# Kernel tuning notes

Hardware: AMD Instinct MI355X
Metric: run time of the kernel (lower is better)

The kernel has to match this reference:

```python
import jax, jax.numpy as jnp
import numpy as np

B, L, D, H, S = 2, 2048, 1024, 16, 4
Dh = D // H
EPS = 1e-5


def setup_inputs() -> dict:
    key = jax.random.key(0)
    ks = jax.random.split(key, 12)
    sc = 0.02
    w = lambda k, shape: (jax.random.normal(k, shape, jnp.float32) * sc)
    M = 2 * S  # number of MHA blocks / dense linears
    inp = {
        "response": jax.random.normal(ks[0], (B, L, D), jnp.float32),
        "mask": jnp.broadcast_to(jnp.tril(jnp.ones((L, L), bool)), (B, L, L)),
        "Wq": w(ks[1], (M, D, D)), "bq": w(ks[2], (M, D)),
        "Wk": w(ks[3], (M, D, D)), "bk": w(ks[4], (M, D)),
        "Wv": w(ks[5], (M, D, D)), "bv": w(ks[6], (M, D)),
        "Wo": w(ks[7], (M, D, D)), "bo": w(ks[8], (M, D)),
        "Wd": w(ks[9], (M, D, D)), "bd": w(ks[10], (M, D)),
    }
    return inp


def _ln(x):
    # fresh LayerNorm(d) with default weight=1, bias=0, eps=1e-5
    m = jnp.mean(x, axis=-1, keepdims=True)
    v = jnp.mean((x - m) ** 2, axis=-1, keepdims=True)
    return (x - m) * jax.lax.rsqrt(v + EPS)


def _linear(x, W, b):
    # torch Linear: x @ W.T + b
    return jnp.einsum('bld,od->blo', x, W) + b


def _mha(x, i, mask, Wq, bq, Wk, bk, Wv, bv, Wo, bo):
    # self-attention: q = k = v = x
    split = lambda y: y.reshape(B, L, H, Dh).transpose(0, 2, 1, 3)  # (B,H,L,Dh)
    q = split(_linear(x, Wq[i], bq[i]))
    k = split(_linear(x, Wk[i], bk[i]))
    v = split(_linear(x, Wv[i], bv[i]))
    scores = jnp.einsum('bhqd,bhkd->bhqk', q, k) / jnp.sqrt(jnp.float32(Dh))
    if mask is not None:
        scores = jnp.where(mask[:, None, :, :], scores, -jnp.inf)
    p = jnp.nan_to_num(jax.nn.softmax(scores, axis=-1))
    o = jnp.einsum('bhqk,bhkd->bhqd', p, v).transpose(0, 2, 1, 3).reshape(B, L, D)
    return _linear(o, Wo[i], bo[i])


def reference(response, mask, Wq, bq, Wk, bk, Wv, bv, Wo, bo, Wd, bd):
    x = response
    for i in range(S):
        # masked self-attention + residual + LN
        x = _ln(x + _mha(x, 2 * i, mask, Wq, bq, Wk, bk, Wv, bv, Wo, bo))
        # encoder-attention sublayer (encMem is None -> unmasked self-attention)
        x = _ln(x + _mha(x, 2 * i + 1, None, Wq, bq, Wk, bk, Wv, bv, Wo, bo))
        # dense: linear[2i](LeakyReLU(linear[2i+1](x)))
        h = jax.nn.leaky_relu(_linear(x, Wd[2 * i + 1], bd[2 * i + 1]), negative_slope=0.01)
        h = _linear(h, Wd[2 * i], bd[2 * i])
        x = _ln(x + h)
    return x
```

## Files before the change

kernel.cpp:

```cpp
#include <hip/hip_runtime.h>
#include <stdint.h>
#include <stddef.h>

typedef __attribute__((ext_vector_type(8))) _Float16 f16x8;
typedef __attribute__((ext_vector_type(4))) _Float16 f16x4;
typedef __attribute__((ext_vector_type(4))) float    f32x4;

#define NB 2
#define NL 2048
#define ND 1024
#define NH 16
#define NROWS (NB*NL)

__device__ __forceinline__ void async16(void* lds, const void* g) {
  __builtin_amdgcn_global_load_lds(
      (const __attribute__((address_space(1))) void*)g,
      (__attribute__((address_space(3))) void*)lds, 16, 0, 0);
}

struct CvtArgs { const float* in[5]; _Float16* out[5]; };

__global__ __launch_bounds__(256) void cvt_all(CvtArgs a, int n8)
{
  const float* in  = a.in[blockIdx.z];
  _Float16*   out  = a.out[blockIdx.z];
  for (int i = blockIdx.x * blockDim.x + threadIdx.x; i < n8;
       i += gridDim.x * blockDim.x) {
    float4 v0 = ((const float4*)in)[2 * i];
    float4 v1 = ((const float4*)in)[2 * i + 1];
    f16x8 o = {(_Float16)v0.x, (_Float16)v0.y, (_Float16)v0.z, (_Float16)v0.w,
               (_Float16)v1.x, (_Float16)v1.y, (_Float16)v1.z, (_Float16)v1.w};
    ((f16x8*)out)[i] = o;
  }
}

__global__ __launch_bounds__(256) void init_x(
    const float* __restrict__ r, _Float16* __restrict__ xh, int n8)
{
  for (int i = blockIdx.x * blockDim.x + threadIdx.x; i < n8;
       i += gridDim.x * blockDim.x) {
    float4 v0 = ((const float4*)r)[2 * i];
    float4 v1 = ((const float4*)r)[2 * i + 1];
    f16x8 o = {(_Float16)v0.x, (_Float16)v0.y, (_Float16)v0.z, (_Float16)v0.w,
               (_Float16)v1.x, (_Float16)v1.y, (_Float16)v1.z, (_Float16)v1.w};
    ((f16x8*)xh)[i] = o;
  }
}

struct GArgs {
  const _Float16* A;
  const _Float16* B[3];
  const float*    bias[3];
  void*           out[3];
  int             mode[3];
  int             ksplit;
};

__global__ __launch_bounds__(256, 2) void gemm_bt(GArgs ga)
{
  __shared__ _Float16 As[2][128 * 64];
  __shared__ _Float16 Bs[2][128 * 64];
  const int tid = threadIdx.x;
  const int w = tid >> 6, l = tid & 63;
  const int ql = l & 15, g = l >> 4;
  const int z = blockIdx.z;
  const int widx = ga.ksplit ? 0 : (blockIdx.x >> 3);
  const _Float16* Bw  = ga.B[widx];
  const float*   bias = ga.bias[widx];
  void*          outp = ga.ksplit ? ga.out[z] : ga.out[widx];
  const int      mode = ga.mode[widx];
  const int kbeg = ga.ksplit ? z * (ND / 2) : 0;
  const int kend = ga.ksplit ? kbeg + ND / 2 : ND;
  const bool dobias = (!ga.ksplit) || (z == 0);
  const int brow = blockIdx.y * 128;
  const int bcol = (blockIdx.x & 7) * 128;
  const int wm = w >> 1, wn = w & 1;
  f32x4 acc[4][4] = {};

  const int srow = w * 32 + (l >> 3);
  const int scol = ((l & 7) ^ (l >> 3)) << 3;
  const _Float16* Ag = ga.A + (size_t)(brow + srow) * ND + scol;
  const _Float16* Bg = Bw   + (size_t)(bcol + srow) * ND + scol;

#define STAGE(buf, k0_)                                                  \
  {                                                                      \
    _Float16* AsW = &As[buf][w * 2048];                                  \
    _Float16* BsW = &Bs[buf][w * 2048];                                  \
    _Pragma("unroll")                                                    \
    for (int i = 0; i < 4; ++i) {                                        \
      async16(AsW + i * 512, Ag + (size_t)i * 8 * ND + (k0_));           \
      async16(BsW + i * 512, Bg + (size_t)i * 8 * ND + (k0_));           \
    }                                                                    \
  }

  STAGE(0, kbeg);
  for (int k0 = kbeg; k0 < kend; k0 += 64) {
    const int cur = ((k0 - kbeg) >> 6) & 1;
    if (k0 + 64 < kend) {
      STAGE(cur ^ 1, k0 + 64);
      asm volatile("s_waitcnt vmcnt(8)" ::: "memory");
    } else {
      asm volatile("s_waitcnt vmcnt(0)" ::: "memory");
    }
    __builtin_amdgcn_s_barrier();
    __builtin_amdgcn_s_setprio(1);
#pragma unroll
    for (int ks = 0; ks < 64; ks += 32) {
      const int cx = (ks + g * 8) ^ ((ql & 7) << 3);
      f16x8 af[4], bf[4];
#pragma unroll
      for (int mi = 0; mi < 4; ++mi)
        af[mi] = *(const f16x8*)&As[cur][(wm * 64 + mi * 16 + ql) * 64 + cx];
#pragma unroll
      for (int nj = 0; nj < 4; ++nj)
        bf[nj] = *(const f16x8*)&Bs[cur][(wn * 64 + nj * 16 + ql) * 64 + cx];
#pragma unroll
      for (int mi = 0; mi < 4; ++mi)
#pragma unroll
        for (int nj = 0; nj < 4; ++nj)
          acc[mi][nj] = __builtin_amdgcn_mfma_f32_16x16x32_f16(
              af[mi], bf[nj], acc[mi][nj], 0, 0, 0);
    }
    __builtin_amdgcn_s_setprio(0);
    asm volatile("s_waitcnt lgkmcnt(0)" ::: "memory");
    __builtin_amdgcn_s_barrier();
  }
#undef STAGE

  const int colb = bcol + wn * 64;
  const int rowb = brow + wm * 64 + g * 4;
  if (mode == 3) {
    _Float16* vt = (_Float16*)outp;
    const int bb = rowb >> 11;
#pragma unroll
    for (int nj = 0; nj < 4; ++nj) {
      const int col = colb + nj * 16 + ql;
      const float bv = bias[col];
      const int hh = col >> 6, d = col & 63;
      _Float16* vrow = vt + ((size_t)((bb * NH + hh) * 64 + d)) * NL;
#pragma unroll
      for (int mi = 0; mi < 4; ++mi) {
        const int krow = (rowb + mi * 16) & (NL - 1);
        f16x4 o;
#pragma unroll
        for (int r = 0; r < 4; ++r) o[r] = (_Float16)(acc[mi][nj][r] + bv);
        *(f16x4*)(vrow + krow) = o;
      }
    }
  } else {
    _Float16* oh = (_Float16*)outp;
#pragma unroll
    for (int nj = 0; nj < 4; ++nj) {
      const int col = colb + nj * 16 + ql;
      const float bv = dobias ? bias[col] : 0.f;
#pragma unroll
      for (int mi = 0; mi < 4; ++mi) {
#pragma unroll
        for (int r = 0; r < 4; ++r) {
          float v = acc[mi][nj][r] + bv;
          if (mode == 2) v = v > 0.f ? v : 0.01f * v;
          oh[(size_t)(rowb + mi * 16 + r) * ND + col] = (_Float16)v;
        }
      }
    }
  }
}

template<bool CAUSAL>
__global__ __launch_bounds__(512, 4) void attn_fwd(
    const _Float16* __restrict__ Q, const _Float16* __restrict__ K,
    const _Float16* __restrict__ Vt, _Float16* __restrict__ O)
{
  __shared__ _Float16 kv[3][2][64 * 64];
  __shared__ unsigned int pls[8][8 * 34];
  const int tid = threadIdx.x;
  const int w = tid >> 6, l = tid & 63;
  const int ql = l & 15, g = l >> 4;
  const int h = blockIdx.y, b = blockIdx.z;
  const int qt = (CAUSAL && b) ? (NL / 128 - 1 - (int)blockIdx.x) : blockIdx.x;
  const int qrow = qt * 128 + w * 16 + ql;

  const _Float16* Qp = Q + (size_t)(b * NL + qrow) * ND + h * 64 + g * 8;
  const f16x8 bq0 = *(const f16x8*)Qp;
  const f16x8 bq1 = *(const f16x8*)(Qp + 32);

  const int srow = w * 8 + (l >> 3);
  const int scol = ((l & 7) ^ (l >> 3)) << 3;
  const _Float16* Kg = K  + ((size_t)(b * NL) + srow) * ND + h * 64 + scol;
  const _Float16* Vg = Vt + ((size_t)((b * NH + h) * 64 + srow)) * NL + scol;

  const int msk  = (ql & 7) << 3;
  const int offA = ql * 64 + ((     g * 8) ^ msk);
  const int offB = ql * 64 + ((32 + g * 8) ^ msk);

  unsigned int* pw = &pls[w][0];
  f32x4 ot[4] = {};
  float s_run = 0.f;
  const int ntiles = CAUSAL ? (qt * 2 + 2) : (NL / 64);
  const float SCL = 0.125f * 1.44269504089f;
  const float M2  = 4.0f * 1.44269504089f;

  async16(&kv[0][0][w * 512], Kg);
  async16(&kv[0][1][w * 512], Vg);

  int cbuf = 0, sbuf = 1;
  for (int kt = 0; kt < ntiles; ++kt) {
    const size_t nk0 = (size_t)((kt + 1 < ntiles) ? kt + 1 : kt) * 64;
    async16(&kv[sbuf][0][w * 512], Kg + nk0 * ND);
    async16(&kv[sbuf][1][w * 512], Vg + nk0);
    asm volatile("s_waitcnt vmcnt(2)" ::: "memory");
    __builtin_amdgcn_s_barrier();

    const _Float16* kb = &kv[cbuf][0][0];
    const _Float16* vb = &kv[cbuf][1][0];
    const int k0 = kt * 64;
    f32x4 st[4] = {};
    __builtin_amdgcn_s_setprio(1);
#pragma unroll
    for (int sub = 0; sub < 4; ++sub) {
      const f16x8 a0 = *(const f16x8*)&kb[sub * 1024 + offA];
      const f16x8 a1 = *(const f16x8*)&kb[sub * 1024 + offB];
      st[sub] = __builtin_amdgcn_mfma_f32_16x16x32_f16(a0, bq0, st[sub], 0, 0, 0);
      st[sub] = __builtin_amdgcn_mfma_f32_16x16x32_f16(a1, bq1, st[sub], 0, 0, 0);
    }
    __builtin_amdgcn_s_setprio(0);
    float ps = 0.f;
    float pv[16];
#pragma unroll
    for (int sub = 0; sub < 4; ++sub)
#pragma unroll
      for (int r = 0; r < 4; ++r) {
        float p = exp2f(__builtin_fmaf(st[sub][r], SCL, -M2));
        if (CAUSAL && (k0 + sub * 16 + g * 4 + r) > qrow) p = 0.f;
        pv[sub * 4 + r] = p;
        ps += p;
      }
    ps += __shfl_xor(ps, 16);
    ps += __shfl_xor(ps, 32);
    s_run += ps;

#pragma unroll
    for (int sub = 0; sub < 2; ++sub) {
      uint2 uu;
      uu.x = __builtin_bit_cast(unsigned int,
                __builtin_amdgcn_cvt_pkrtz(pv[sub * 4 + 0], pv[sub * 4 + 1]));
      uu.y = __builtin_bit_cast(unsigned int,
                __builtin_amdgcn_cvt_pkrtz(pv[sub * 4 + 2], pv[sub * 4 + 3]));
      *(uint2*)&pw[(sub * 4 + g) * 34 + 2 * ql] = uu;
    }
    {
      uint2 lo = *(const uint2*)&pw[(2 * g    ) * 34 + 2 * ql];
      uint2 hi = *(const uint2*)&pw[(2 * g + 1) * 34 + 2 * ql];
      uint4 ui; ui.x = lo.x; ui.y = lo.y; ui.z = hi.x; ui.w = hi.y;
      const f16x8 pf = __builtin_bit_cast(f16x8, ui);
      __builtin_amdgcn_s_setprio(1);
#pragma unroll
      for (int dt = 0; dt < 4; ++dt) {
        const f16x8 vf = *(const f16x8*)&vb[dt * 1024 + offA];
        ot[dt] = __builtin_amdgcn_mfma_f32_16x16x32_f16(vf, pf, ot[dt], 0, 0, 0);
      }
      __builtin_amdgcn_s_setprio(0);
    }
#pragma unroll
    for (int sub = 2; sub < 4; ++sub) {
      uint2 uu;
      uu.x = __builtin_bit_cast(unsigned int,
                __builtin_amdgcn_cvt_pkrtz(pv[sub * 4 + 0], pv[sub * 4 + 1]));
      uu.y = __builtin_bit_cast(unsigned int,
                __builtin_amdgcn_cvt_pkrtz(pv[sub * 4 + 2], pv[sub * 4 + 3]));
      *(uint2*)&pw[((sub - 2) * 4 + g) * 34 + 2 * ql] = uu;
    }
    {
      uint2 lo = *(const uint2*)&pw[(2 * g    ) * 34 + 2 * ql];
      uint2 hi = *(const uint2*)&pw[(2 * g + 1) * 34 + 2 * ql];
      uint4 ui; ui.x = lo.x; ui.y = lo.y; ui.z = hi.x; ui.w = hi.y;
      const f16x8 pf = __builtin_bit_cast(f16x8, ui);
      __builtin_amdgcn_s_setprio(1);
#pragma unroll
      for (int dt = 0; dt < 4; ++dt) {
        const f16x8 vf = *(const f16x8*)&vb[dt * 1024 + offB];
        ot[dt] = __builtin_amdgcn_mfma_f32_16x16x32_f16(vf, pf, ot[dt], 0, 0, 0);
      }
      __builtin_amdgcn_s_setprio(0);
    }
    cbuf = sbuf;
    sbuf = sbuf + 1 == 3 ? 0 : sbuf + 1;
  }

  const float inv = 1.f / s_run;
#pragma unroll
  for (int dt = 0; dt < 4; ++dt) {
    f16x4 o;
#pragma unroll
    for (int r = 0; r < 4; ++r) o[r] = (_Float16)(ot[dt][r] * inv);
    *(f16x4*)(O + (size_t)(b * NL + qrow) * ND + h * 64 + dt * 16 + g * 4) = o;
  }
}

template<bool FINAL>
__global__ __launch_bounds__(256) void resid_ln(
    const _Float16* __restrict__ xh_in, const _Float16* __restrict__ d0,
    const _Float16* __restrict__ d1,
    _Float16* __restrict__ xh_out, float* __restrict__ xf)
{
  const int row = blockIdx.x, tid = threadIdx.x;
  const f16x4 xv = ((const f16x4*)(xh_in + (size_t)row * ND))[tid];
  const f16x4 v0 = ((const f16x4*)(d0 + (size_t)row * ND))[tid];
  const f16x4 v1 = ((const f16x4*)(d1 + (size_t)row * ND))[tid];
  const float a = (float)xv[0] + (float)v0[0] + (float)v1[0];
  const float b = (float)xv[1] + (float)v0[1] + (float)v1[1];
  const float c = (float)xv[2] + (float)v0[2] + (float)v1[2];
  const float d = (float)xv[3] + (float)v0[3] + (float)v1[3];
  float s = a + b + c + d;
  float ss = a * a + b * b + c * c + d * d;
#pragma unroll
  for (int m = 1; m < 64; m <<= 1) {
    s  += __shfl_xor(s, m);
    ss += __shfl_xor(ss, m);
  }
  __shared__ float red[8];
  if ((tid & 63) == 0) { red[tid >> 6] = s; red[4 + (tid >> 6)] = ss; }
  __syncthreads();
  const float S  = red[0] + red[1] + red[2] + red[3];
  const float SS = red[4] + red[5] + red[6] + red[7];
  const float mean = S * (1.0f / ND);
  const float var  = SS * (1.0f / ND) - mean * mean;
  const float rstd = rsqrtf(fmaxf(var, 0.f) + 1e-5f);
  const float ya = (a - mean) * rstd, yb = (b - mean) * rstd;
  const float yc = (c - mean) * rstd, yd = (d - mean) * rstd;
  if (FINAL) {
    float4 y; y.x = ya; y.y = yb; y.z = yc; y.w = yd;
    ((float4*)(xf + (size_t)row * ND))[tid] = y;
  } else {
    f16x4 yh = {(_Float16)ya, (_Float16)yb, (_Float16)yc, (_Float16)yd};
    ((f16x4*)(xh_out + (size_t)row * ND))[tid] = yh;
  }
}

extern "C" void kernel_launch(void* const* d_in, const int* in_sizes, int n_in,
                              void* d_out, int out_size, void* d_ws, size_t ws_size,
                              hipStream_t stream)
{
  (void)in_sizes; (void)n_in; (void)out_size; (void)ws_size;
  const float* response = (const float*)d_in[0];
  const float* Wq = (const float*)d_in[2];
  const float* bq = (const float*)d_in[3];
  const float* Wk = (const float*)d_in[4];
  const float* bk = (const float*)d_in[5];
  const float* Wv = (const float*)d_in[6];
  const float* bv = (const float*)d_in[7];
  const float* Wo = (const float*)d_in[8];
  const float* bo = (const float*)d_in[9];
  const float* Wd = (const float*)d_in[10];
  const float* bd = (const float*)d_in[11];
  float* xf = (float*)d_out;

  const size_t MB = 1024 * 1024;
  char* p = (char*)d_ws;
  _Float16* Wq_h = (_Float16*)(p + 0 * MB);
  _Float16* Wk_h = (_Float16*)(p + 16 * MB);
  _Float16* Wv_h = (_Float16*)(p + 32 * MB);
  _Float16* Wo_h = (_Float16*)(p + 48 * MB);
  _Float16* Wd_h = (_Float16*)(p + 64 * MB);
  _Float16* xh   = (_Float16*)(p + 80 * MB);
  _Float16* Qh   = (_Float16*)(p + 88 * MB);
  _Float16* Kh   = (_Float16*)(p + 96 * MB);
  _Float16* Vth  = (_Float16*)(p + 104 * MB);
  _Float16* Oh   = (_Float16*)(p + 112 * MB);
  _Float16* h1   = Qh;
  _Float16* t0   = (_Float16*)(p + 96 * MB);
  _Float16* t1   = (_Float16*)(p + 104 * MB);

  const int wn8 = 8 * 1024 * 1024 / 8;
  CvtArgs ca = { { Wq, Wk, Wv, Wo, Wd }, { Wq_h, Wk_h, Wv_h, Wo_h, Wd_h } };
  cvt_all<<<dim3(512, 1, 5), 256, 0, stream>>>(ca, wn8);
  init_x<<<1024, 256, 0, stream>>>(response, xh, NROWS * ND / 8);

  const dim3 g3(24, NROWS / 128, 1);
  const dim3 gs(8, NROWS / 128, 2);
  const dim3 gf(8, NROWS / 128, 1);
  const dim3 agrid(NL / 128, NH, NB);

  for (int i = 0; i < 4; ++i) {
    for (int sub = 0; sub < 2; ++sub) {
      const int m = 2 * i + sub;
      const size_t wo = (size_t)m * MB;
      const size_t bf = (size_t)m * 1024;
      GArgs qkv = { xh,
                    { Wq_h + wo, Wk_h + wo, Wv_h + wo },
                    { bq + bf, bk + bf, bv + bf },
                    { Qh, Kh, Vth }, { 0, 0, 3 }, 0 };
      gemm_bt<<<g3, 256, 0, stream>>>(qkv);
      if (sub == 0) attn_fwd<true ><<<agrid, 512, 0, stream>>>(Qh, Kh, Vth, Oh);
      else          attn_fwd<false><<<agrid, 512, 0, stream>>>(Qh, Kh, Vth, Oh);
      GArgs oprj = { Oh,
                     { Wo_h + wo, nullptr, nullptr },
                     { bo + bf, nullptr, nullptr },
                     { t0, t1, nullptr }, { 0, 0, 0 }, 1 };
      gemm_bt<<<gs, 256, 0, stream>>>(oprj);
      resid_ln<false><<<NROWS, 256, 0, stream>>>(xh, t0, t1, xh, nullptr);
    }
    const size_t w1 = (size_t)(2 * i + 1) * MB, b1 = (size_t)(2 * i + 1) * 1024;
    const size_t w0 = (size_t)(2 * i) * MB,     b0 = (size_t)(2 * i) * 1024;
    GArgs f1 = { xh,
                 { Wd_h + w1, nullptr, nullptr },
                 { bd + b1, nullptr, nullptr },
                 { h1, nullptr, nullptr }, { 2, 0, 0 }, 0 };
    gemm_bt<<<gf, 256, 0, stream>>>(f1);
    GArgs f2 = { h1,
                 { Wd_h + w0, nullptr, nullptr },
                 { bd + b0, nullptr, nullptr },
                 { t0, t1, nullptr }, { 0, 0, 0 }, 1 };
    gemm_bt<<<gs, 256, 0, stream>>>(f2);
    if (i == 3) resid_ln<true ><<<NROWS, 256, 0, stream>>>(xh, t0, t1, nullptr, xf);
    else        resid_ln<false><<<NROWS, 256, 0, stream>>>(xh, t0, t1, xh, nullptr);
  }
}
```

Before: 1.194 ms.

## Fuse fp32-to-fp16 weight conversion into GEMM B-tile staging

Removes the separate cvt_all kernel that converted all five fp32 weight stacks to fp16 up front. The GEMM now loads fp32 weights into registers, converts them, and writes the swizzled fp16 tile into LDS, while the activation tile still uses async global-to-LDS loads. This avoids writing and rereading 80MB of fp16 weights and saves a launch. In exchange each GEMM reads twice the weight bytes and does register conversion and LDS stores inside the pipelined loop, which may cost overlap or occupancy.

```diff
diff --git a/kernel.cpp b/kernel.cpp
--- a/kernel.cpp
+++ b/kernel.cpp
@@ -16,22 +16,6 @@
   __builtin_amdgcn_global_load_lds(
       (const __attribute__((address_space(1))) void*)g,
       (__attribute__((address_space(3))) void*)lds, 16, 0, 0);
-}
-
-struct CvtArgs { const float* in[5]; _Float16* out[5]; };
-
-__global__ __launch_bounds__(256) void cvt_all(CvtArgs a, int n8)
-{
-  const float* in  = a.in[blockIdx.z];
-  _Float16*   out  = a.out[blockIdx.z];
-  for (int i = blockIdx.x * blockDim.x + threadIdx.x; i < n8;
-       i += gridDim.x * blockDim.x) {
-    float4 v0 = ((const float4*)in)[2 * i];
-    float4 v1 = ((const float4*)in)[2 * i + 1];
-    f16x8 o = {(_Float16)v0.x, (_Float16)v0.y, (_Float16)v0.z, (_Float16)v0.w,
-               (_Float16)v1.x, (_Float16)v1.y, (_Float16)v1.z, (_Float16)v1.w};
-    ((f16x8*)out)[i] = o;
-  }
 }
 
 __global__ __launch_bounds__(256) void init_x(
@@ -49,7 +33,7 @@
 
 struct GArgs {
   const _Float16* A;
-  const _Float16* B[3];
+  const float*    B[3];
   const float*    bias[3];
   void*           out[3];
   int             mode[3];
@@ -65,7 +49,7 @@
   const int ql = l & 15, g = l >> 4;
   const int z = blockIdx.z;
   const int widx = ga.ksplit ? 0 : (blockIdx.x >> 3);
-  const _Float16* Bw  = ga.B[widx];
+  const float*   Bw   = ga.B[widx];
   const float*   bias = ga.bias[widx];
   void*          outp = ga.ksplit ? ga.out[z] : ga.out[widx];
   const int      mode = ga.mode[widx];
@@ -77,31 +61,73 @@
   const int wm = w >> 1, wn = w & 1;
   f32x4 acc[4][4] = {};
 
-  const int srow = w * 32 + (l >> 3);
-  const int scol = ((l & 7) ^ (l >> 3)) << 3;
-  const _Float16* Ag = ga.A + (size_t)(brow + srow) * ND + scol;
-  const _Float16* Bg = Bw   + (size_t)(bcol + srow) * ND + scol;
-
-#define STAGE(buf, k0_)                                                  \
+  const int rsub = l >> 3;
+  const int csub = l & 7;
+  const int swz  = (csub ^ rsub) << 3;
+  const _Float16* Ag = ga.A + (size_t)(brow + w * 32 + rsub) * ND + swz;
+  const float*    Bg = Bw   + (size_t)(bcol + w * 32 + rsub) * ND + csub * 8;
+  const int wrow = w * 32 + rsub;
+
+  float4 b0, b1, b2, b3, b4, b5, b6, b7;
+
+#define LOAD_B(k0_)                                                      \
+  {                                                                      \
+    b0 = *(const float4*)(Bg + 0 * 8 * ND + (k0_));                      \
+    b1 = *(const float4*)(Bg + 0 * 8 * ND + (k0_) + 4);                  \
+    b2 = *(const float4*)(Bg + 1 * 8 * ND + (k0_));                      \
+    b3 = *(const float4*)(Bg + 1 * 8 * ND + (k0_) + 4);                  \
+    b4 = *(const float4*)(Bg + 2 * 8 * ND + (k0_));                      \
+    b5 = *(const float4*)(Bg + 2 * 8 * ND + (k0_) + 4);                  \
+    b6 = *(const float4*)(Bg + 3 * 8 * ND + (k0_));                      \
+    b7 = *(const float4*)(Bg + 3 * 8 * ND + (k0_) + 4);                  \
+  }
+
+#define STAGE_A(buf, k0_)                                                \
   {                                                                      \
     _Float16* AsW = &As[buf][w * 2048];                                  \
-    _Float16* BsW = &Bs[buf][w * 2048];                                  \
     _Pragma("unroll")                                                    \
-    for (int i = 0; i < 4; ++i) {                                        \
-      async16(AsW + i * 512, Ag + (size_t)i * 8 * ND + (k0_));           \
-      async16(BsW + i * 512, Bg + (size_t)i * 8 * ND + (k0_));           \
-    }                                                                    \
-  }
-
-  STAGE(0, kbeg);
+    for (int i2 = 0; i2 < 4; ++i2)                                       \
+      async16(AsW + i2 * 512, Ag + (size_t)i2 * 8 * ND + (k0_));         \
+  }
+
+#define CVT_B(buf)                                                       \
+  {                                                                      \
+    f16x8 h0 = {(_Float16)b0.x, (_Float16)b0.y, (_Float16)b0.z,          \
+                (_Float16)b0.w, (_Float16)b1.x, (_Float16)b1.y,          \
+                (_Float16)b1.z, (_Float16)b1.w};                         \
+    f16x8 h1 = {(_Float16)b2.x, (_Float16)b2.y, (_Float16)b2.z,          \
+                (_Float16)b2.w, (_Float16)b3.x, (_Float16)b3.y,          \
+                (_Float16)b3.z, (_Float16)b3.w};                         \
+    f16x8 h2 = {(_Float16)b4.x, (_Float16)b4.y, (_Float16)b4.z,          \
+                (_Float16)b4.w, (_Float16)b5.x, (_Float16)b5.y,          \
+                (_Float16)b5.z, (_Float16)b5.w};                         \
+    f16x8 h3 = {(_Float16)b6.x, (_Float16)b6.y, (_Float16)b6.z,          \
+                (_Float16)b6.w, (_Float16)b7.x, (_Float16)b7.y,          \
+                (_Float16)b7.z, (_Float16)b7.w};                         \
+    *(f16x8*)&Bs[buf][(wrow +  0) * 64 + swz] = h0;                      \
+    *(f16x8*)&Bs[buf][(wrow +  8) * 64 + swz] = h1;                      \
+    *(f16x8*)&Bs[buf][(wrow + 16) * 64 + swz] = h2;                      \
+    *(f16x8*)&Bs[buf][(wrow + 24) * 64 + swz] = h3;                      \
+  }
+
+  LOAD_B(kbeg);
+  asm volatile("" ::: "memory");
+  STAGE_A(0, kbeg);
+  asm volatile("s_waitcnt vmcnt(4)" ::: "memory");
+  CVT_B(0);
+
   for (int k0 = kbeg; k0 < kend; k0 += 64) {
     const int cur = ((k0 - kbeg) >> 6) & 1;
     if (k0 + 64 < kend) {
-      STAGE(cur ^ 1, k0 + 64);
-      asm volatile("s_waitcnt vmcnt(8)" ::: "memory");
+      LOAD_B(k0 + 64);
+      asm volatile("" ::: "memory");
+      STAGE_A(cur ^ 1, k0 + 64);
+      asm volatile("s_waitcnt vmcnt(4)" ::: "memory");
+      CVT_B(cur ^ 1);
     } else {
       asm volatile("s_waitcnt vmcnt(0)" ::: "memory");
     }
+    asm volatile("s_waitcnt lgkmcnt(0)" ::: "memory");
     __builtin_amdgcn_s_barrier();
     __builtin_amdgcn_s_setprio(1);
 #pragma unroll
@@ -125,7 +151,9 @@
     asm volatile("s_waitcnt lgkmcnt(0)" ::: "memory");
     __builtin_amdgcn_s_barrier();
   }
-#undef STAGE
+#undef LOAD_B
+#undef STAGE_A
+#undef CVT_B
 
   const int colb = bcol + wn * 64;
   const int rowb = brow + wm * 64 + g * 4;
@@ -357,23 +385,15 @@
 
   const size_t MB = 1024 * 1024;
   char* p = (char*)d_ws;
-  _Float16* Wq_h = (_Float16*)(p + 0 * MB);
-  _Float16* Wk_h = (_Float16*)(p + 16 * MB);
-  _Float16* Wv_h = (_Float16*)(p + 32 * MB);
-  _Float16* Wo_h = (_Float16*)(p + 48 * MB);
-  _Float16* Wd_h = (_Float16*)(p + 64 * MB);
-  _Float16* xh   = (_Float16*)(p + 80 * MB);
-  _Float16* Qh   = (_Float16*)(p + 88 * MB);
-  _Float16* Kh   = (_Float16*)(p + 96 * MB);
-  _Float16* Vth  = (_Float16*)(p + 104 * MB);
-  _Float16* Oh   = (_Float16*)(p + 112 * MB);
+  _Float16* xh   = (_Float16*)(p + 0 * MB);
+  _Float16* Qh   = (_Float16*)(p + 8 * MB);
+  _Float16* Kh   = (_Float16*)(p + 16 * MB);
+  _Float16* Vth  = (_Float16*)(p + 24 * MB);
+  _Float16* Oh   = (_Float16*)(p + 32 * MB);
   _Float16* h1   = Qh;
-  _Float16* t0   = (_Float16*)(p + 96 * MB);
-  _Float16* t1   = (_Float16*)(p + 104 * MB);
-
-  const int wn8 = 8 * 1024 * 1024 / 8;
-  CvtArgs ca = { { Wq, Wk, Wv, Wo, Wd }, { Wq_h, Wk_h, Wv_h, Wo_h, Wd_h } };
-  cvt_all<<<dim3(512, 1, 5), 256, 0, stream>>>(ca, wn8);
+  _Float16* t0   = Kh;
+  _Float16* t1   = Vth;
+
   init_x<<<1024, 256, 0, stream>>>(response, xh, NROWS * ND / 8);
 
   const dim3 g3(24, NROWS / 128, 1);
@@ -387,14 +407,14 @@
       const size_t wo = (size_t)m * MB;
       const size_t bf = (size_t)m * 1024;
       GArgs qkv = { xh,
-                    { Wq_h + wo, Wk_h + wo, Wv_h + wo },
+                    { Wq + wo, Wk + wo, Wv + wo },
                     { bq + bf, bk + bf, bv + bf },
                     { Qh, Kh, Vth }, { 0, 0, 3 }, 0 };
       gemm_bt<<<g3, 256, 0, stream>>>(qkv);
       if (sub == 0) attn_fwd<true ><<<agrid, 512, 0, stream>>>(Qh, Kh, Vth, Oh);
       else          attn_fwd<false><<<agrid, 512, 0, stream>>>(Qh, Kh, Vth, Oh);
       GArgs oprj = { Oh,
-                     { Wo_h + wo, nullptr, nullptr },
+                     { Wo + wo, nullptr, nullptr },
                      { bo + bf, nullptr, nullptr },
                      { t0, t1, nullptr }, { 0, 0, 0 }, 1 };
       gemm_bt<<<gs, 256, 0, stream>>>(oprj);
@@ -403,12 +423,12 @@
     const size_t w1 = (size_t)(2 * i + 1) * MB, b1 = (size_t)(2 * i + 1) * 1024;
     const size_t w0 = (size_t)(2 * i) * MB,     b0 = (size_t)(2 * i) * 1024;
     GArgs f1 = { xh,
-                 { Wd_h + w1, nullptr, nullptr },
+                 { Wd + w1, nullptr, nullptr },
                  { bd + b1, nullptr, nullptr },
                  { h1, nullptr, nullptr }, { 2, 0, 0 }, 0 };
     gemm_bt<<<gf, 256, 0, stream>>>(f1);
     GArgs f2 = { h1,
-                 { Wd_h + w0, nullptr, nullptr },
+                 { Wd + w0, nullptr, nullptr },
                  { bd + b0, nullptr, nullptr },
                  { t0, t1, nullptr }, { 0, 0, 0 }, 1 };
     gemm_bt<<<gs, 256, 0, stream>>>(f2);
```

Result: slower. 1.326 ms (+11.1%).
